# Kernel optimization log

Measured on AMD Instinct MI355X. Metric: run time of the kernel, lower is better.

Reference implementation:

```python
import jax, jax.numpy as jnp
import numpy as np

H = 10          # heads
DIMS = [4, 256, 256, 256, 256, 256, 256, 2]  # model_param
B = 32768
OBS_X, OBS_Y, R = 0.0, 7.0, 4.0
L1, L2 = 3.0, 3.0


def _linear_params(key, din, dout, n=H):
    kw, kb = jax.random.split(key)
    s = 1.0 / np.sqrt(din)
    W = jax.random.uniform(kw, (n, dout, din), jnp.float32, -s, s)
    b = jax.random.uniform(kb, (n, dout), jnp.float32, -s, s)
    return W, b


def setup_inputs() -> dict:
    key = jax.random.key(0)
    ks = jax.random.split(key, 16)
    inp = {
        "x": jax.random.normal(ks[0], (B, DIMS[0]), jnp.float32),
        "sgn": 1,
        "wt": jnp.ones((H,), jnp.float32),
        "mean": jnp.zeros((DIMS[0],), jnp.float32),
        "std": jnp.ones((DIMS[0],), jnp.float32),
        "mean_label": jnp.zeros((DIMS[7],), jnp.float32),
        "std_label": jnp.ones((DIMS[7],), jnp.float32),
    }
    inp["W1"], inp["b1"] = _linear_params(ks[1], DIMS[0], DIMS[1])
    inp["W2"], inp["b2"] = _linear_params(ks[2], DIMS[1], DIMS[2])
    inp["W31"], inp["b31"] = _linear_params(ks[3], DIMS[2], DIMS[3])
    inp["W32"], inp["b32"] = _linear_params(ks[4], DIMS[2], DIMS[4])
    inp["W41"], inp["b41"] = _linear_params(ks[5], DIMS[3], DIMS[5])
    inp["W42"], inp["b42"] = _linear_params(ks[6], DIMS[4], DIMS[6])
    inp["W51"], inp["b51"] = _linear_params(ks[7], DIMS[5], DIMS[7])
    inp["W52"], inp["b52"] = _linear_params(ks[8], DIMS[6], DIMS[7])
    return inp


def _forward(x, W1, b1, W2, b2, W31, b31, W32, b32, W41, b41, W42, b42,
             W51, b51, W52, b52, wt, mean, std, mean_label, std_label):
    relu = jax.nn.relu
    x0 = x * std + mean                                   # de-normalized state [B,4]

    # Stacked per-head MLP (heads axis h)
    x1 = relu(jnp.einsum('bi,hoi->hbo', x, W1) + b1[:, None, :])
    x2 = relu(jnp.einsum('hbi,hoi->hbo', x1, W2) + b2[:, None, :])
    x31 = relu(jnp.einsum('hbi,hoi->hbo', x2, W31) + b31[:, None, :])
    x32 = relu(jnp.einsum('hbi,hoi->hbo', x2, W32) + b32[:, None, :])
    x41 = relu(jnp.einsum('hbi,hoi->hbo', x31, W41) + b41[:, None, :])
    x42 = relu(jnp.einsum('hbi,hoi->hbo', x32, W42) + b42[:, None, :])
    x51 = jnp.einsum('hbi,hoi->hbo', x41, W51) + b51[:, None, :]       # [H,B,2] QP linear cost
    x52 = 4.0 * jax.nn.sigmoid(jnp.einsum('hbi,hoi->hbo', x42, W52) + b52[:, None, :])  # [H,B,2] CBF gains

    # CBF geometric quantities (shared across heads)
    t1, w1, t2, w2 = x0[:, 0], x0[:, 1], x0[:, 2], x0[:, 3]
    s1, s2, c1, c2 = jnp.sin(t1), jnp.sin(t2), jnp.cos(t1), jnp.cos(t2)
    px = L1 * c1 + L2 * c2 - OBS_X
    py = L1 * s1 + L2 * s2 - OBS_Y
    vx = -L1 * s1 * w1 - L2 * s2 * w2
    vy = L1 * c1 * w1 + L2 * c2 * w2
    barrier = px ** 2 + py ** 2 - R ** 2
    b_dot = 2 * px * vx + 2 * py * vy
    Lf2b = (2 * vx ** 2 + 2 * vy ** 2
            + 2 * px * (-L1 * c1 * w1 ** 2 - L2 * c2 * w2 ** 2)
            + 2 * py * (-L1 * s1 * w1 ** 2 - L2 * s2 * w2 ** 2))
    LgLfbu1 = 2 * px * (-L1 * s1) + 2 * py * (L1 * c1)
    LgLfbu2 = 2 * px * (-L2 * s2) + 2 * py * (L2 * c2)
    g = jnp.stack([-LgLfbu1, -LgLfbu2], axis=-1)          # [B,2] constraint row

    # h uses head-0's x52[:,0] for every head (self.x52 caching in the torch code)
    a0 = x52[0, :, 0]                                     # [B]
    b_i = x52[:, :, 1]                                    # [H,B]
    h = Lf2b[None] + (a0[None] + b_i) * b_dot[None] + a0[None] * b_i * barrier[None]  # [H,B]

    # QP min 0.5 u'u + p'u  s.t. g.u <= h  -> closed-form halfspace projection
    u_unc = -x51                                          # [H,B,2]
    gg = jnp.sum(g * g, axis=-1)                          # [B]
    viol = jnp.einsum('hbc,bc->hb', u_unc, g) - h         # [H,B]
    lam = jnp.maximum(viol, 0.0) / gg[None]               # active-set multiplier
    u = u_unc - lam[..., None] * g[None]                  # [H,B,2]
    u = (u - mean_label) / std_label

    w = jax.nn.softmax(wt)                                # exp(wt)/sum(exp(wt))
    return jnp.einsum('h,hbc->bc', w, u)                  # [B,2]


def reference(x, sgn, wt, mean, std, mean_label, std_label,
              W1, b1, W2, b2, W31, b31, W32, b32, W41, b41, W42, b42,
              W51, b51, W52, b52):
    return _forward(x, W1, b1, W2, b2, W31, b31, W32, b32, W41, b41,
                    W42, b42, W51, b51, W52, b52, wt, mean, std,
                    mean_label, std_label)
```

## Files before the change

### kernel.cpp

```cpp
#include <hip/hip_runtime.h>
#include <hip/hip_bf16.h>

typedef __attribute__((ext_vector_type(8)))  short bf16x8_t;
typedef __attribute__((ext_vector_type(16))) float f32x16_t;
typedef __attribute__((ext_vector_type(4)))  float f32x4_t;

#define HN 10
#define BN 32768
#define DH 256
#define MT 64

#define KS17 17
#define HE17   (KS17*8*64*8)
#define ARRE17 (HN*HE17)

#define OFF_A     0
#define OFF_B     32768
#define OFF_S5    65536
#define SMEM_BYTES 66560

#define MFMA32 __builtin_amdgcn_mfma_f32_32x32x16_bf16

__device__ __forceinline__ unsigned swzoff(int row, int colb) {
  return (unsigned)(row * 512 + (colb ^ ((row & 31) << 4)));
}

__device__ __forceinline__ unsigned short f2bf(float v) {
  __hip_bfloat16 hb = __float2bfloat16(v);
  return *reinterpret_cast<unsigned short*>(&hb);
}
__device__ __forceinline__ unsigned pk2bf(float lo, float hi_) {
  return (unsigned)f2bf(lo) | ((unsigned)f2bf(hi_) << 16);
}

struct WPtrs { const float* w[5]; const float* b[5]; };

extern "C" __global__ void pack_big(WPtrs p, unsigned short* __restrict__ dst)
{
  int g = blockIdx.x * blockDim.x + threadIdx.x;
  if (g >= 5 * HN * KS17 * 8 * 64) return;
  int lane = g & 63; int t = g >> 6;
  int nt = t & 7; t >>= 3;
  int ks = t % KS17; t /= KS17;
  int h = t % HN;
  int a = t / HN;
  int col = nt * 32 + (lane & 31);
  int hi = lane >> 5;
  unsigned short* d = dst + (size_t)a * ARRE17 + (size_t)h * HE17
                    + ((ks * 8 + nt) * 64 + lane) * 8;
  if (ks < 16) {
    const float* src = p.w[a] + (size_t)h * 65536 + col * 256 + ks * 16 + hi * 8;
    #pragma unroll
    for (int j = 0; j < 8; ++j) d[j] = f2bf(src[j]);
  } else {
    float bv = p.b[a][(size_t)h * 256 + col];
    #pragma unroll
    for (int j = 0; j < 8; ++j) d[j] = (hi == 0 && j == 0) ? f2bf(bv) : (unsigned short)0;
  }
}

extern "C" __global__ void pack_w5(const float* __restrict__ w51, const float* __restrict__ w52,
                                   const float* __restrict__ b51, const float* __restrict__ b52,
                                   unsigned short* __restrict__ dst)
{
  int g = blockIdx.x * blockDim.x + threadIdx.x;
  if (g >= 2 * HN * KS17 * 64) return;
  int lane = g & 63; int t = g >> 6;
  int ks = t % KS17; t /= KS17;
  int h = t % HN;
  int br = t / HN;
  const float* w = br ? w52 : w51;
  const float* b = br ? b52 : b51;
  int col = lane & 31;
  int hi = lane >> 5;
  unsigned short* d = dst + ((size_t)(br * HN + h) * KS17 + ks) * 512 + lane * 8;
  if (ks < 16) {
    int k = ks * 16 + hi * 8;
    #pragma unroll
    for (int j = 0; j < 8; ++j) {
      float v = (col < 2) ? w[(size_t)h * 512 + col * 256 + k + j] : 0.f;
      d[j] = f2bf(v);
    }
  } else {
    float bv = (col < 2) ? b[(size_t)h * 2 + col] : 0.f;
    #pragma unroll
    for (int j = 0; j < 8; ++j) d[j] = (hi == 0 && j == 0) ? f2bf(bv) : (unsigned short)0;
  }
}

extern "C" __global__ void pack_w1(const float* __restrict__ w1, const float* __restrict__ b1,
                                   unsigned short* __restrict__ dst)
{
  int g = blockIdx.x * blockDim.x + threadIdx.x;
  if (g >= HN * 8 * 64) return;
  int lane = g & 63; int t = g >> 6;
  int nt = t & 7;
  int h = t >> 3;
  int col = nt * 32 + (lane & 31);
  int hi = lane >> 5;
  unsigned short* d = dst + (size_t)h * 4096 + ((size_t)nt * 64 + lane) * 8;
  #pragma unroll
  for (int j = 0; j < 8; ++j) {
    int k = hi * 8 + j;
    float v = 0.f;
    if (k < 4)       v = w1[(size_t)h * 1024 + col * 4 + k];
    else if (k == 4) v = b1[(size_t)h * 256 + col];
    d[j] = f2bf(v);
  }
}


__device__ __forceinline__ void write_actT(char* sout, const f32x16_t acc[2][2],
                                           int lane, int wave)
{
  const int r31 = lane & 31, hi = lane >> 5;
  #pragma unroll
  for (int mt = 0; mt < 2; ++mt) {
    const int row = mt * 32 + r31;
    #pragma unroll
    for (int nt = 0; nt < 2; ++nt) {
      #pragma unroll
      for (int g = 0; g < 4; ++g) {
        const int col0 = (wave * 2 + nt) * 32 + 8 * g + 4 * hi;
        unsigned w0 = pk2bf(fmaxf(acc[mt][nt][4 * g + 0], 0.f),
                            fmaxf(acc[mt][nt][4 * g + 1], 0.f));
        unsigned w1 = pk2bf(fmaxf(acc[mt][nt][4 * g + 2], 0.f),
                            fmaxf(acc[mt][nt][4 * g + 3], 0.f));
        unsigned long long pk = (unsigned long long)w0 | ((unsigned long long)w1 << 32);
        *(unsigned long long*)(sout + swzoff(row, col0 * 2)) = pk;
      }
    }
  }
}

template<bool INPLACE>
__device__ __forceinline__ void gemm_pp(const char* sin, char* sout,
                                        const unsigned short* __restrict__ wl,
                                        int lane, int wave, bf16x8_t ones)
{
  const int r31 = lane & 31, hi = lane >> 5;
  f32x16_t acc[2][2];
  #pragma unroll
  for (int mt = 0; mt < 2; ++mt)
    #pragma unroll
    for (int nt = 0; nt < 2; ++nt)
      #pragma unroll
      for (int i = 0; i < 16; ++i) acc[mt][nt][i] = 0.f;

  const char* wb = (const char*)wl + (size_t)(wave * 2) * 1024 + (size_t)lane * 16;
  bf16x8_t c0[2], c1[2], c2[2];
  #pragma unroll
  for (int nt = 0; nt < 2; ++nt) {
    c0[nt] = *(const bf16x8_t*)(wb + nt * 1024);
    c1[nt] = *(const bf16x8_t*)(wb + 8192 + nt * 1024);
  }
  #pragma unroll
  for (int ks = 0; ks < KS17; ++ks) {
    if (ks < KS17 - 2) {
      #pragma unroll
      for (int nt = 0; nt < 2; ++nt)
        c2[nt] = *(const bf16x8_t*)(wb + (ks + 2) * 8192 + nt * 1024);
    }
    bf16x8_t a[2];
    #pragma unroll
    for (int mt = 0; mt < 2; ++mt)
      a[mt] = (ks < 16)
        ? *(const bf16x8_t*)(sin + swzoff(mt * 32 + r31, ks * 32 + hi * 16))
        : ones;
    #pragma unroll
    for (int mt = 0; mt < 2; ++mt) {
      acc[mt][0] = MFMA32(c0[0], a[mt], acc[mt][0], 0, 0, 0);
      acc[mt][1] = MFMA32(c0[1], a[mt], acc[mt][1], 0, 0, 0);
    }
    #pragma unroll
    for (int nt = 0; nt < 2; ++nt) { c0[nt] = c1[nt]; c1[nt] = c2[nt]; }
  }
  if (INPLACE) __syncthreads();
  write_actT(sout, acc, lane, wave);
  __syncthreads();
}

__device__ __forceinline__ void final_pp(const char* sin, float* s5,
                                         const unsigned short* __restrict__ w5,
                                         float* __restrict__ wsout,
                                         int row0, int tid, int lane, int wave,
                                         bf16x8_t ones)
{
  const int r31 = lane & 31, hi = lane >> 5;
  if (wave < 2) {
    const int mt = wave;
    f32x16_t acc;
    #pragma unroll
    for (int i = 0; i < 16; ++i) acc[i] = 0.f;
    #pragma unroll
    for (int ks = 0; ks < KS17; ++ks) {
      bf16x8_t a = (ks < 16)
        ? *(const bf16x8_t*)(sin + swzoff(mt * 32 + r31, ks * 32 + hi * 16))
        : ones;
      bf16x8_t b = *(const bf16x8_t*)(w5 + (size_t)(ks * 64 + lane) * 8);
      acc = MFMA32(a, b, acc, 0, 0, 0);
    }
    if (r31 < 2) {
      #pragma unroll
      for (int r = 0; r < 16; ++r) {
        int row = mt * 32 + (r & 3) + 8 * (r >> 2) + 4 * hi;
        s5[row * 2 + r31] = acc[r];
      }
    }
  }
  __syncthreads();
  if (tid < 128) {
    int row = tid >> 1, c = tid & 1;
    wsout[(size_t)(row0 + row) * 2 + c] = s5[row * 2 + c];
  }
}

extern "C" __global__ __launch_bounds__(256, 2)
void abnet_main(const float* __restrict__ x,
                const unsigned short* __restrict__ wpk,
                const unsigned short* __restrict__ w5pk,
                const unsigned short* __restrict__ w1pk,
                float* __restrict__ ws51, float* __restrict__ ws52)
{
  extern __shared__ char smem[];
  char*  bufA = smem + OFF_A;
  char*  bufB = smem + OFF_B;
  float* s5   = (float*)(smem + OFF_S5);

  const int tid  = threadIdx.x;
  const int lane = tid & 63, wave = tid >> 6;
  const int L  = (blockIdx.x & 7) * 640 + (blockIdx.x >> 3);
  const int rt = L & 511;
  const int h  = L >> 9;
  const int row0 = rt * MT;

  const int r31 = lane & 31, hi = lane >> 5;

  bf16x8_t ones;
  #pragma unroll
  for (int j = 0; j < 8; ++j) ones[j] = 0;
  if (hi == 0) ones[0] = (short)0x3F80;

  {
    const char* w1b = (const char*)(w1pk + (size_t)h * 4096)
                    + (size_t)(wave * 2) * 1024 + (size_t)lane * 16;
    bf16x8_t wf[2];
    #pragma unroll
    for (int nt = 0; nt < 2; ++nt) wf[nt] = *(const bf16x8_t*)(w1b + nt * 1024);
    f32x16_t acc[2][2];
    #pragma unroll
    for (int mt = 0; mt < 2; ++mt)
      #pragma unroll
      for (int nt = 0; nt < 2; ++nt)
        #pragma unroll
        for (int i = 0; i < 16; ++i) acc[mt][nt][i] = 0.f;
    #pragma unroll
    for (int mt = 0; mt < 2; ++mt) {
      int row = row0 + mt * 32 + r31;
      f32x4_t xv = *(const f32x4_t*)(x + (size_t)row * 4);
      bf16x8_t af;
      #pragma unroll
      for (int j = 0; j < 8; ++j) {
        short v = 0;
        if (hi == 0) {
          if (j < 4)       v = (short)f2bf(xv[j]);
          else if (j == 4) v = (short)0x3F80;
        }
        af[j] = v;
      }
      acc[mt][0] = MFMA32(wf[0], af, acc[mt][0], 0, 0, 0);
      acc[mt][1] = MFMA32(wf[1], af, acc[mt][1], 0, 0, 0);
    }
    write_actT(bufA, acc, lane, wave);
    __syncthreads();
  }

  const unsigned short* W2  = wpk + (size_t)h * HE17;
  const unsigned short* W31 = wpk + 1 * (size_t)ARRE17 + (size_t)h * HE17;
  const unsigned short* W32 = wpk + 2 * (size_t)ARRE17 + (size_t)h * HE17;
  const unsigned short* W41 = wpk + 3 * (size_t)ARRE17 + (size_t)h * HE17;
  const unsigned short* W42 = wpk + 4 * (size_t)ARRE17 + (size_t)h * HE17;

  gemm_pp<false>(bufA, bufB, W2, lane, wave, ones);

  gemm_pp<false>(bufB, bufA, W31, lane, wave, ones);
  gemm_pp<true >(bufA, bufA, W41, lane, wave, ones);
  final_pp(bufA, s5, w5pk + (size_t)h * (KS17 * 512),
           ws51 + (size_t)h * BN * 2, row0, tid, lane, wave, ones);

  gemm_pp<false>(bufB, bufA, W32, lane, wave, ones);
  gemm_pp<true >(bufA, bufA, W42, lane, wave, ones);
  final_pp(bufA, s5, w5pk + (size_t)(HN + h) * (KS17 * 512),
           ws52 + (size_t)h * BN * 2, row0, tid, lane, wave, ones);
}

extern "C" __global__ __launch_bounds__(256)
void abnet_epi(const float* __restrict__ x, const float* __restrict__ wt,
               const float* __restrict__ mean, const float* __restrict__ stdv,
               const float* __restrict__ mlab, const float* __restrict__ slab,
               const float* __restrict__ ws51, const float* __restrict__ ws52,
               float* __restrict__ out)
{
  const int row = blockIdx.x * 256 + threadIdx.x;
  f32x4_t xr = *(const f32x4_t*)(x + (size_t)row * 4);
  float t1  = xr[0] * stdv[0] + mean[0];
  float w1v = xr[1] * stdv[1] + mean[1];
  float t2  = xr[2] * stdv[2] + mean[2];
  float w2v = xr[3] * stdv[3] + mean[3];
  float s1, c1, s2, c2;
  sincosf(t1, &s1, &c1);
  sincosf(t2, &s2, &c2);
  float px = 3.f * c1 + 3.f * c2;
  float py = 3.f * s1 + 3.f * s2 - 7.f;
  float vx = -3.f * s1 * w1v - 3.f * s2 * w2v;
  float vy =  3.f * c1 * w1v + 3.f * c2 * w2v;
  float e_bar  = px * px + py * py - 16.f;
  float e_bdot = 2.f * (px * vx + py * vy);
  float e_lf2b = 2.f * vx * vx + 2.f * vy * vy
               + 2.f * px * (-3.f * c1 * w1v * w1v - 3.f * c2 * w2v * w2v)
               + 2.f * py * (-3.f * s1 * w1v * w1v - 3.f * s2 * w2v * w2v);
  float e_g1 = 6.f * (px * s1 - py * c1);
  float e_g2 = 6.f * (px * s2 - py * c2);
  float e_ggi = 1.f / (e_g1 * e_g1 + e_g2 * e_g2);

  float m = wt[0];
  for (int i = 1; i < HN; ++i) m = fmaxf(m, wt[i]);
  float s = 0.f;
  for (int i = 0; i < HN; ++i) s += __expf(wt[i] - m);
  float sm_inv = 1.f / s;
  float ml0 = mlab[0], ml1 = mlab[1];
  float isl0 = 1.f / slab[0], isl1 = 1.f / slab[1];

  float a0r = 4.f / (1.f + __expf(-ws52[(size_t)row * 2 + 0]));
  float accu0 = 0.f, accu1 = 0.f;
  for (int h = 0; h < HN; ++h) {
    float u1 = -ws51[((size_t)h * BN + row) * 2 + 0];
    float u2 = -ws51[((size_t)h * BN + row) * 2 + 1];
    float bi = 4.f / (1.f + __expf(-ws52[((size_t)h * BN + row) * 2 + 1]));
    float hv   = e_lf2b + (a0r + bi) * e_bdot + a0r * bi * e_bar;
    float viol = u1 * e_g1 + u2 * e_g2 - hv;
    float lam  = fmaxf(viol, 0.f) * e_ggi;
    float uu1 = u1 - lam * e_g1;
    float uu2 = u2 - lam * e_g2;
    float whv = __expf(wt[h] - m) * sm_inv;
    accu0 += whv * (uu1 - ml0) * isl0;
    accu1 += whv * (uu2 - ml1) * isl1;
  }
  float2 o; o.x = accu0; o.y = accu1;
  *(float2*)(out + (size_t)row * 2) = o;
}

extern "C" void kernel_launch(void* const* d_in, const int* in_sizes, int n_in,
                              void* d_out, int out_size, void* d_ws, size_t ws_size,
                              hipStream_t stream)
{
  const float* x    = (const float*)d_in[0];
  const float* wt   = (const float*)d_in[2];
  const float* mean = (const float*)d_in[3];
  const float* stdv = (const float*)d_in[4];
  const float* mlab = (const float*)d_in[5];
  const float* slab = (const float*)d_in[6];
  const float* W1   = (const float*)d_in[7];
  const float* b1   = (const float*)d_in[8];
  WPtrs wp;
  wp.w[0] = (const float*)d_in[9];
  wp.w[1] = (const float*)d_in[11];
  wp.w[2] = (const float*)d_in[13];
  wp.w[3] = (const float*)d_in[15];
  wp.w[4] = (const float*)d_in[17];
  wp.b[0] = (const float*)d_in[10];
  wp.b[1] = (const float*)d_in[12];
  wp.b[2] = (const float*)d_in[14];
  wp.b[3] = (const float*)d_in[16];
  wp.b[4] = (const float*)d_in[18];
  const float* W51 = (const float*)d_in[19];
  const float* b51 = (const float*)d_in[20];
  const float* W52 = (const float*)d_in[21];
  const float* b52 = (const float*)d_in[22];

  char* wsb = (char*)d_ws;
  unsigned short* wpk  = (unsigned short*)wsb;
  unsigned short* w5pk = (unsigned short*)(wsb + 6963200);
  unsigned short* w1pk = (unsigned short*)(wsb + 7311360);
  float* ws51 = (float*)(wsb + 7393280);
  float* ws52 = (float*)(wsb + 10014720);

  hipLaunchKernelGGL(pack_big, dim3(1700), dim3(256), 0, stream, wp, wpk);
  hipLaunchKernelGGL(pack_w5,  dim3(85),   dim3(256), 0, stream, W51, W52, b51, b52, w5pk);
  hipLaunchKernelGGL(pack_w1,  dim3(20),   dim3(256), 0, stream, W1, b1, w1pk);

  (void)hipFuncSetAttribute(reinterpret_cast<const void*>(abnet_main),
                            hipFuncAttributeMaxDynamicSharedMemorySize, SMEM_BYTES);
  hipLaunchKernelGGL(abnet_main, dim3(512 * HN), dim3(256), SMEM_BYTES, stream,
                     x, wpk, w5pk, w1pk, ws51, ws52);
  hipLaunchKernelGGL(abnet_epi, dim3(BN / 256), dim3(256), 0, stream,
                     x, wt, mean, stdv, mlab, slab, ws51, ws52, (float*)d_out);
}
```

Baseline: 263.9 us.

## Prefetch next layer's weights across GEMM stages and deepen weight pipeline

Each GEMM stage now preloads the first two k-slices of the next layer's weights before its barrier, so weight loads overlap the activation write-back and sync. The in-loop weight prefetch distance grows from two to three k-steps using a 4-slot rotating register buffer. The MFMA loop runs at raised wave priority, and __syncthreads is replaced with a barrier that waits only on LDS counters, so outstanding global loads are not drained. The cost is more live VGPRs, which could hurt occupancy under the 2-blocks-per-SM launch bound.

```diff
diff --git a/kernel.cpp b/kernel.cpp
--- a/kernel.cpp
+++ b/kernel.cpp
@@ -20,6 +20,8 @@
 #define SMEM_BYTES 66560
 
 #define MFMA32 __builtin_amdgcn_mfma_f32_32x32x16_bf16
+
+#define BAR_LDS() asm volatile("s_waitcnt lgkmcnt(0)\ns_barrier" ::: "memory")
 
 __device__ __forceinline__ unsigned swzoff(int row, int colb) {
   return (unsigned)(row * 512 + (colb ^ ((row & 31) << 4)));
@@ -110,6 +112,15 @@
 }
 
 
+struct Pre { bf16x8_t f[4]; };
+
+__device__ __forceinline__ void preload(const char* wb, Pre& p) {
+  p.f[0] = *(const bf16x8_t*)(wb);
+  p.f[1] = *(const bf16x8_t*)(wb + 1024);
+  p.f[2] = *(const bf16x8_t*)(wb + 8192);
+  p.f[3] = *(const bf16x8_t*)(wb + 8192 + 1024);
+}
+
 __device__ __forceinline__ void write_actT(char* sout, const f32x16_t acc[2][2],
                                            int lane, int wave)
 {
@@ -135,7 +146,8 @@
 
 template<bool INPLACE>
 __device__ __forceinline__ void gemm_pp(const char* sin, char* sout,
-                                        const unsigned short* __restrict__ wl,
+                                        const char* wb, Pre& cur,
+                                        const char* wbn, Pre& nxt,
                                         int lane, int wave, bf16x8_t ones)
 {
   const int r31 = lane & 31, hi = lane >> 5;
@@ -147,19 +159,18 @@
       #pragma unroll
       for (int i = 0; i < 16; ++i) acc[mt][nt][i] = 0.f;
 
-  const char* wb = (const char*)wl + (size_t)(wave * 2) * 1024 + (size_t)lane * 16;
-  bf16x8_t c0[2], c1[2], c2[2];
-  #pragma unroll
-  for (int nt = 0; nt < 2; ++nt) {
-    c0[nt] = *(const bf16x8_t*)(wb + nt * 1024);
-    c1[nt] = *(const bf16x8_t*)(wb + 8192 + nt * 1024);
-  }
+  bf16x8_t c[4][2];
+  c[0][0] = cur.f[0]; c[0][1] = cur.f[1];
+  c[1][0] = cur.f[2]; c[1][1] = cur.f[3];
+  c[2][0] = *(const bf16x8_t*)(wb + 2 * 8192);
+  c[2][1] = *(const bf16x8_t*)(wb + 2 * 8192 + 1024);
+
+  __builtin_amdgcn_s_setprio(1);
   #pragma unroll
   for (int ks = 0; ks < KS17; ++ks) {
-    if (ks < KS17 - 2) {
-      #pragma unroll
-      for (int nt = 0; nt < 2; ++nt)
-        c2[nt] = *(const bf16x8_t*)(wb + (ks + 2) * 8192 + nt * 1024);
+    if (ks + 3 < KS17) {
+      c[(ks + 3) & 3][0] = *(const bf16x8_t*)(wb + (ks + 3) * 8192);
+      c[(ks + 3) & 3][1] = *(const bf16x8_t*)(wb + (ks + 3) * 8192 + 1024);
     }
     bf16x8_t a[2];
     #pragma unroll
@@ -169,15 +180,17 @@
         : ones;
     #pragma unroll
     for (int mt = 0; mt < 2; ++mt) {
-      acc[mt][0] = MFMA32(c0[0], a[mt], acc[mt][0], 0, 0, 0);
-      acc[mt][1] = MFMA32(c0[1], a[mt], acc[mt][1], 0, 0, 0);
-    }
-    #pragma unroll
-    for (int nt = 0; nt < 2; ++nt) { c0[nt] = c1[nt]; c1[nt] = c2[nt]; }
-  }
-  if (INPLACE) __syncthreads();
+      acc[mt][0] = MFMA32(c[ks & 3][0], a[mt], acc[mt][0], 0, 0, 0);
+      acc[mt][1] = MFMA32(c[ks & 3][1], a[mt], acc[mt][1], 0, 0, 0);
+    }
+  }
+  __builtin_amdgcn_s_setprio(0);
+
+  if (wbn) preload(wbn, nxt);
+
+  if (INPLACE) BAR_LDS();
   write_actT(sout, acc, lane, wave);
-  __syncthreads();
+  BAR_LDS();
 }
 
 __device__ __forceinline__ void final_pp(const char* sin, float* s5,
@@ -208,7 +221,7 @@
       }
     }
   }
-  __syncthreads();
+  BAR_LDS();
   if (tid < 128) {
     int row = tid >> 1, c = tid & 1;
     wsout[(size_t)(row0 + row) * 2 + c] = s5[row * 2 + c];
@@ -241,9 +254,18 @@
   for (int j = 0; j < 8; ++j) ones[j] = 0;
   if (hi == 0) ones[0] = (short)0x3F80;
 
+  const size_t woff = (size_t)(wave * 2) * 1024 + (size_t)lane * 16;
+  const char* W2w  = (const char*)(wpk + (size_t)h * HE17) + woff;
+  const char* W31w = (const char*)(wpk + 1 * (size_t)ARRE17 + (size_t)h * HE17) + woff;
+  const char* W32w = (const char*)(wpk + 2 * (size_t)ARRE17 + (size_t)h * HE17) + woff;
+  const char* W41w = (const char*)(wpk + 3 * (size_t)ARRE17 + (size_t)h * HE17) + woff;
+  const char* W42w = (const char*)(wpk + 4 * (size_t)ARRE17 + (size_t)h * HE17) + woff;
+
+  Pre preA, preB;
+  preload(W2w, preA);
+
   {
-    const char* w1b = (const char*)(w1pk + (size_t)h * 4096)
-                    + (size_t)(wave * 2) * 1024 + (size_t)lane * 16;
+    const char* w1b = (const char*)(w1pk + (size_t)h * 4096) + woff;
     bf16x8_t wf[2];
     #pragma unroll
     for (int nt = 0; nt < 2; ++nt) wf[nt] = *(const bf16x8_t*)(w1b + nt * 1024);
@@ -272,24 +294,18 @@
       acc[mt][1] = MFMA32(wf[1], af, acc[mt][1], 0, 0, 0);
     }
     write_actT(bufA, acc, lane, wave);
-    __syncthreads();
-  }
-
-  const unsigned short* W2  = wpk + (size_t)h * HE17;
-  const unsigned short* W31 = wpk + 1 * (size_t)ARRE17 + (size_t)h * HE17;
-  const unsigned short* W32 = wpk + 2 * (size_t)ARRE17 + (size_t)h * HE17;
-  const unsigned short* W41 = wpk + 3 * (size_t)ARRE17 + (size_t)h * HE17;
-  const unsigned short* W42 = wpk + 4 * (size_t)ARRE17 + (size_t)h * HE17;
-
-  gemm_pp<false>(bufA, bufB, W2, lane, wave, ones);
-
-  gemm_pp<false>(bufB, bufA, W31, lane, wave, ones);
-  gemm_pp<true >(bufA, bufA, W41, lane, wave, ones);
+    BAR_LDS();
+  }
+
+  gemm_pp<false>(bufA, bufB, W2w,  preA, W31w, preB, lane, wave, ones);
+
+  gemm_pp<false>(bufB, bufA, W31w, preB, W41w, preA, lane, wave, ones);
+  gemm_pp<true >(bufA, bufA, W41w, preA, W32w, preB, lane, wave, ones);
   final_pp(bufA, s5, w5pk + (size_t)h * (KS17 * 512),
            ws51 + (size_t)h * BN * 2, row0, tid, lane, wave, ones);
 
-  gemm_pp<false>(bufB, bufA, W32, lane, wave, ones);
-  gemm_pp<true >(bufA, bufA, W42, lane, wave, ones);
+  gemm_pp<false>(bufB, bufA, W32w, preB, W42w, preA, lane, wave, ones);
+  gemm_pp<true >(bufA, bufA, W42w, preA, nullptr, preB, lane, wave, ones);
   final_pp(bufA, s5, w5pk + (size_t)(HN + h) * (KS17 * 512),
            ws52 + (size_t)h * BN * 2, row0, tid, lane, wave, ones);
 }
```

Measured after the change: 266.4 us. About the same (+1.0%).

## Single LDS buffer with register-saved x2 activations to fit three blocks per CU

Applied to the files above, without the earlier changes.

The second LDS activation buffer is removed. The layer-2 output is kept in registers (packed bf16) and written back to LDS before the second branch, so all GEMMs run in place on one 32KB buffer. LDS use drops to about 33KB and launch bounds are raised to 3 blocks per CU. __syncthreads is replaced with an explicit lgkmcnt wait plus s_barrier. The saved values cost 32 registers per thread under a tighter register budget, which risks spills and adds an extra barrier in every layer.

```diff
diff --git a/kernel.cpp b/kernel.cpp
--- a/kernel.cpp
+++ b/kernel.cpp
@@ -15,11 +15,12 @@
 #define ARRE17 (HN*HE17)
 
 #define OFF_A     0
-#define OFF_B     32768
-#define OFF_S5    65536
-#define SMEM_BYTES 66560
+#define OFF_S5    32768
+#define SMEM_BYTES 33280
 
 #define MFMA32 __builtin_amdgcn_mfma_f32_32x32x16_bf16
+
+#define BAR_LDS() asm volatile("s_waitcnt lgkmcnt(0)\ns_barrier" ::: "memory")
 
 __device__ __forceinline__ unsigned swzoff(int row, int colb) {
   return (unsigned)(row * 512 + (colb ^ ((row & 31) << 4)));
@@ -110,8 +111,9 @@
 }
 
 
+template<bool SAVE>
 __device__ __forceinline__ void write_actT(char* sout, const f32x16_t acc[2][2],
-                                           int lane, int wave)
+                                           unsigned sv[2][2][8], int lane, int wave)
 {
   const int r31 = lane & 31, hi = lane >> 5;
   #pragma unroll
@@ -126,6 +128,7 @@
                             fmaxf(acc[mt][nt][4 * g + 1], 0.f));
         unsigned w1 = pk2bf(fmaxf(acc[mt][nt][4 * g + 2], 0.f),
                             fmaxf(acc[mt][nt][4 * g + 3], 0.f));
+        if (SAVE) { sv[mt][nt][2 * g] = w0; sv[mt][nt][2 * g + 1] = w1; }
         unsigned long long pk = (unsigned long long)w0 | ((unsigned long long)w1 << 32);
         *(unsigned long long*)(sout + swzoff(row, col0 * 2)) = pk;
       }
@@ -133,9 +136,9 @@
   }
 }
 
-template<bool INPLACE>
-__device__ __forceinline__ void gemm_pp(const char* sin, char* sout,
-                                        const unsigned short* __restrict__ wl,
+template<bool SAVE>
+__device__ __forceinline__ void gemm_ip(char* buf, const char* wb,
+                                        unsigned sv[2][2][8],
                                         int lane, int wave, bf16x8_t ones)
 {
   const int r31 = lane & 31, hi = lane >> 5;
@@ -147,7 +150,6 @@
       #pragma unroll
       for (int i = 0; i < 16; ++i) acc[mt][nt][i] = 0.f;
 
-  const char* wb = (const char*)wl + (size_t)(wave * 2) * 1024 + (size_t)lane * 16;
   bf16x8_t c0[2], c1[2], c2[2];
   #pragma unroll
   for (int nt = 0; nt < 2; ++nt) {
@@ -165,7 +167,7 @@
     #pragma unroll
     for (int mt = 0; mt < 2; ++mt)
       a[mt] = (ks < 16)
-        ? *(const bf16x8_t*)(sin + swzoff(mt * 32 + r31, ks * 32 + hi * 16))
+        ? *(const bf16x8_t*)(buf + swzoff(mt * 32 + r31, ks * 32 + hi * 16))
         : ones;
     #pragma unroll
     for (int mt = 0; mt < 2; ++mt) {
@@ -175,9 +177,9 @@
     #pragma unroll
     for (int nt = 0; nt < 2; ++nt) { c0[nt] = c1[nt]; c1[nt] = c2[nt]; }
   }
-  if (INPLACE) __syncthreads();
-  write_actT(sout, acc, lane, wave);
-  __syncthreads();
+  BAR_LDS();
+  write_actT<SAVE>(buf, acc, sv, lane, wave);
+  BAR_LDS();
 }
 
 __device__ __forceinline__ void final_pp(const char* sin, float* s5,
@@ -208,14 +210,14 @@
       }
     }
   }
-  __syncthreads();
+  BAR_LDS();
   if (tid < 128) {
     int row = tid >> 1, c = tid & 1;
     wsout[(size_t)(row0 + row) * 2 + c] = s5[row * 2 + c];
   }
 }
 
-extern "C" __global__ __launch_bounds__(256, 2)
+extern "C" __global__ __launch_bounds__(256, 3)
 void abnet_main(const float* __restrict__ x,
                 const unsigned short* __restrict__ wpk,
                 const unsigned short* __restrict__ w5pk,
@@ -224,7 +226,6 @@
 {
   extern __shared__ char smem[];
   char*  bufA = smem + OFF_A;
-  char*  bufB = smem + OFF_B;
   float* s5   = (float*)(smem + OFF_S5);
 
   const int tid  = threadIdx.x;
@@ -241,9 +242,17 @@
   for (int j = 0; j < 8; ++j) ones[j] = 0;
   if (hi == 0) ones[0] = (short)0x3F80;
 
+  const size_t woff = (size_t)(wave * 2) * 1024 + (size_t)lane * 16;
+  const char* W2w  = (const char*)(wpk + (size_t)h * HE17) + woff;
+  const char* W31w = (const char*)(wpk + 1 * (size_t)ARRE17 + (size_t)h * HE17) + woff;
+  const char* W32w = (const char*)(wpk + 2 * (size_t)ARRE17 + (size_t)h * HE17) + woff;
+  const char* W41w = (const char*)(wpk + 3 * (size_t)ARRE17 + (size_t)h * HE17) + woff;
+  const char* W42w = (const char*)(wpk + 4 * (size_t)ARRE17 + (size_t)h * HE17) + woff;
+
+  unsigned sv[2][2][8];
+
   {
-    const char* w1b = (const char*)(w1pk + (size_t)h * 4096)
-                    + (size_t)(wave * 2) * 1024 + (size_t)lane * 16;
+    const char* w1b = (const char*)(w1pk + (size_t)h * 4096) + woff;
     bf16x8_t wf[2];
     #pragma unroll
     for (int nt = 0; nt < 2; ++nt) wf[nt] = *(const bf16x8_t*)(w1b + nt * 1024);
@@ -271,25 +280,37 @@
       acc[mt][0] = MFMA32(wf[0], af, acc[mt][0], 0, 0, 0);
       acc[mt][1] = MFMA32(wf[1], af, acc[mt][1], 0, 0, 0);
     }
-    write_actT(bufA, acc, lane, wave);
-    __syncthreads();
-  }
-
-  const unsigned short* W2  = wpk + (size_t)h * HE17;
-  const unsigned short* W31 = wpk + 1 * (size_t)ARRE17 + (size_t)h * HE17;
-  const unsigned short* W32 = wpk + 2 * (size_t)ARRE17 + (size_t)h * HE17;
-  const unsigned short* W41 = wpk + 3 * (size_t)ARRE17 + (size_t)h * HE17;
-  const unsigned short* W42 = wpk + 4 * (size_t)ARRE17 + (size_t)h * HE17;
-
-  gemm_pp<false>(bufA, bufB, W2, lane, wave, ones);
-
-  gemm_pp<false>(bufB, bufA, W31, lane, wave, ones);
-  gemm_pp<true >(bufA, bufA, W41, lane, wave, ones);
+    write_actT<false>(bufA, acc, sv, lane, wave);
+    BAR_LDS();
+  }
+
+  gemm_ip<true >(bufA, W2w,  sv, lane, wave, ones);
+
+  gemm_ip<false>(bufA, W31w, sv, lane, wave, ones);
+  gemm_ip<false>(bufA, W41w, sv, lane, wave, ones);
   final_pp(bufA, s5, w5pk + (size_t)h * (KS17 * 512),
            ws51 + (size_t)h * BN * 2, row0, tid, lane, wave, ones);
 
-  gemm_pp<false>(bufB, bufA, W32, lane, wave, ones);
-  gemm_pp<true >(bufA, bufA, W42, lane, wave, ones);
+  {
+    #pragma unroll
+    for (int mt = 0; mt < 2; ++mt) {
+      const int row = mt * 32 + r31;
+      #pragma unroll
+      for (int nt = 0; nt < 2; ++nt) {
+        #pragma unroll
+        for (int g = 0; g < 4; ++g) {
+          const int col0 = (wave * 2 + nt) * 32 + 8 * g + 4 * hi;
+          unsigned long long pk = (unsigned long long)sv[mt][nt][2 * g]
+                                | ((unsigned long long)sv[mt][nt][2 * g + 1] << 32);
+          *(unsigned long long*)(bufA + swzoff(row, col0 * 2)) = pk;
+        }
+      }
+    }
+    BAR_LDS();
+  }
+
+  gemm_ip<false>(bufA, W32w, sv, lane, wave, ones);
+  gemm_ip<false>(bufA, W42w, sv, lane, wave, ones);
   final_pp(bufA, s5, w5pk + (size_t)(HN + h) * (KS17 * 512),
            ws52 + (size_t)h * BN * 2, row0, tid, lane, wave, ones);
 }
```

Result: faster. 250.8 us (-5.0%).
